# Kernel tuning notes

Measured on AMD Instinct MI355X. Metric: run time of the kernel, lower is better.

## Reference

```python
import jax, jax.numpy as jnp
import numpy as np

N_NODES = 100000
N_EDGES = 1600000
IN_DIM = 128
HID_DIM = 64
OUT_DIM = 1


def setup_inputs() -> dict:
    key = jax.random.key(0)
    k = jax.random.split(key, 8)
    x = jax.random.normal(k[0], (N_NODES, IN_DIM), dtype=jnp.float32)
    edge_index = jax.random.randint(k[1], (2, N_EDGES), 0, N_NODES, dtype=jnp.int64)
    # GCNConv layer 1: weight [IN, HID], bias [HID] (glorot-ish scale)
    W1 = jax.random.normal(k[2], (IN_DIM, HID_DIM), dtype=jnp.float32) / np.sqrt(IN_DIM)
    b1 = jnp.zeros((HID_DIM,), dtype=jnp.float32)
    W2 = jax.random.normal(k[3], (HID_DIM, HID_DIM), dtype=jnp.float32) / np.sqrt(HID_DIM)
    b2 = jnp.zeros((HID_DIM,), dtype=jnp.float32)
    Wfc = jax.random.normal(k[4], (HID_DIM, OUT_DIM), dtype=jnp.float32) / np.sqrt(HID_DIM)
    bfc = jnp.zeros((OUT_DIM,), dtype=jnp.float32)
    return {"x": x, "edge_index": edge_index, "W1": W1, "b1": b1,
            "W2": W2, "b2": b2, "Wfc": Wfc, "bfc": bfc}


def _gcn_norm(edge_index, n_nodes):
    # PyG GCNConv default: add self-loops, symmetric normalization.
    src, dst = edge_index[0], edge_index[1]
    loop = jnp.arange(n_nodes, dtype=src.dtype)
    src = jnp.concatenate([src, loop])
    dst = jnp.concatenate([dst, loop])
    deg = jax.ops.segment_sum(jnp.ones_like(dst, dtype=jnp.float32), dst,
                              num_segments=n_nodes)
    deg_isqrt = jax.lax.rsqrt(deg)  # deg >= 1 thanks to self-loops
    norm = deg_isqrt[src] * deg_isqrt[dst]  # [E+N]
    return src, dst, norm


def _gcn_conv(x, src, dst, norm, W, b, n_nodes):
    h = x @ W                      # [N, D_out] dense transform first (D_out <= D_in)
    msg = h[src] * norm[:, None]   # gather + normalize  [E+N, D_out]
    out = jax.ops.segment_sum(msg, dst, num_segments=n_nodes)  # scatter-add
    return out + b


def reference(x, edge_index, W1, b1, W2, b2, Wfc, bfc):
    n = x.shape[0]
    src, dst, norm = _gcn_norm(edge_index, n)
    h = jax.nn.relu(_gcn_conv(x, src, dst, norm, W1, b1, n))
    h = jax.nn.relu(_gcn_conv(h, src, dst, norm, W2, b2, n))
    return h @ Wfc + bfc  # [N, 1]
```

## Files before the change

kernel.cpp:

```cpp
#include <hip/hip_runtime.h>


#define IN_DIM 128
#define HID 64
#define B1 256
#define MAXNC 512

typedef unsigned int uint;
typedef unsigned short ushort;
typedef __attribute__((ext_vector_type(8))) short short8;
typedef __attribute__((ext_vector_type(4))) float f32x4;

__device__ inline uint pack_bf16x2(float a, float b) {
    uint ua = __builtin_bit_cast(uint, a);
    uint ub = __builtin_bit_cast(uint, b);
    ua += 0x7fffu + ((ua >> 16) & 1u);
    ub += 0x7fffu + ((ub >> 16) & 1u);
    return (ua >> 16) | (ub & 0xffff0000u);
}
__device__ inline float bf_lo(uint g) { return __builtin_bit_cast(float, g << 16); }
__device__ inline float bf_hi(uint g) { return __builtin_bit_cast(float, g & 0xffff0000u); }
__device__ inline uint rne_hi_bits(float a) {
    uint u = __builtin_bit_cast(uint, a);
    return (u + 0x7fffu + ((u >> 16) & 1u)) & 0xffff0000u;
}
__device__ inline float bitf(uint u) { return __builtin_bit_cast(float, u); }

__global__ __launch_bounds__(512) void hist1(const int* __restrict__ dst,
                                             int* __restrict__ ghist,
                                             int E, int NC, int chunk) {
    __shared__ int h[MAXNC];
    int t = threadIdx.x, blk = blockIdx.x;
    if (t < NC) h[t] = 0;
    __syncthreads();
    int s = blk * chunk, e = min(E, s + chunk);
    for (int i = s + t; i < e; i += 512) atomicAdd(&h[dst[i] >> 8], 1);
    __syncthreads();
    if (t < NC) ghist[(size_t)t * B1 + blk] = h[t];
}

__global__ __launch_bounds__(512) void scan_p12(const int* __restrict__ a,
                                                int* __restrict__ boff,
                                                int* __restrict__ row_off,
                                                int M, int N,
                                                const float* __restrict__ W1f,
                                                const float* __restrict__ W2f,
                                                ushort* __restrict__ w1h,
                                                ushort* __restrict__ w1l,
                                                ushort* __restrict__ w2h,
                                                ushort* __restrict__ w2l) {
    int t = threadIdx.x;
    {
        int c = t & 63;
        int kb1 = (t >> 6) * 16;
#pragma unroll 4
        for (int kk = 0; kk < 16; ++kk) {
            int k = kb1 + kk;
            float v = W1f[k * 64 + c];
            uint rh = rne_hi_bits(v);
            w1h[c * 128 + k] = (ushort)(rh >> 16);
            w1l[c * 128 + k] = (ushort)(rne_hi_bits(v - bitf(rh)) >> 16);
        }
        int kb2 = (t >> 6) * 8;
#pragma unroll 4
        for (int kk = 0; kk < 8; ++kk) {
            int k = kb2 + kk;
            float v = W2f[k * 64 + c];
            uint rh = rne_hi_bits(v);
            w2h[c * 64 + k] = (ushort)(rh >> 16);
            w2l[c * 64 + k] = (ushort)(rne_hi_bits(v - bitf(rh)) >> 16);
        }
    }
    const int nb = (M + 255) >> 8;
    int v = 0;
    if (t < nb) {
        int base = t * 256, end = min(M, base + 256);
        const int4* p4 = (const int4*)(a + base);
        int4 sa = make_int4(0, 0, 0, 0);
        int q4 = (end - base) >> 2;
        for (int k = 0; k < q4; ++k) {
            int4 q = p4[k];
            sa.x += q.x; sa.y += q.y; sa.z += q.z; sa.w += q.w;
        }
        v = sa.x + sa.y + sa.z + sa.w;
        for (int r = base + (q4 << 2); r < end; ++r) v += a[r];
    }
    __shared__ int s[512];
    s[t] = v;
    __syncthreads();
#pragma unroll
    for (int o = 1; o < 512; o <<= 1) {
        int add = (t >= o) ? s[t - o] : 0;
        __syncthreads();
        s[t] += add;
        __syncthreads();
    }
    if (t < nb) boff[t] = s[t] - v;
    if (t == nb - 1) row_off[N] = s[t];
}

__global__ __launch_bounds__(256) void scan_p3(int* __restrict__ a,
                                               const int* __restrict__ boff, int M) {
    __shared__ int s[256];
    int i = blockIdx.x * 256 + threadIdx.x;
    int t = threadIdx.x;
    int d = (i < M) ? a[i] : 0;
    s[t] = d;
    __syncthreads();
#pragma unroll
    for (int o = 1; o < 256; o <<= 1) {
        int add = (t >= o) ? s[t - o] : 0;
        __syncthreads();
        s[t] += add;
        __syncthreads();
    }
    if (i < M) a[i] = s[t] - d + boff[blockIdx.x];
}

__global__ __launch_bounds__(512) void scatter1(const int* __restrict__ src,
                                                const int* __restrict__ dst,
                                                const int* __restrict__ goff,
                                                uint* __restrict__ pairs,
                                                int E, int NC, int chunk) {
    __shared__ int cur[MAXNC];
    int t = threadIdx.x, blk = blockIdx.x;
    if (t < NC) cur[t] = goff[(size_t)t * B1 + blk];
    __syncthreads();
    int s = blk * chunk, e = min(E, s + chunk);
    for (int i = s + t; i < e; i += 512) {
        int d = dst[i];
        int p = atomicAdd(&cur[d >> 8], 1);
        pairs[p] = ((uint)src[i] << 8) | (uint)(d & 255);
    }
}

__global__ __launch_bounds__(256) void build_csr(const uint* __restrict__ pairs,
                                                 const int* __restrict__ goff,
                                                 int* __restrict__ row_off,
                                                 float* __restrict__ disqrt,
                                                 int* __restrict__ col,
                                                 int E, int NC, int N) {
    __shared__ int h[256], cur[256];
    __shared__ int ws[4], wsoff[4];
    int b = blockIdx.x, t = threadIdx.x;
    int base = goff[(size_t)b * B1];
    int next = (b + 1 < NC) ? goff[(size_t)(b + 1) * B1] : E;
    h[t] = 0;
    __syncthreads();
    for (int i = base + t; i < next; i += 256)
        atomicAdd(&h[pairs[i] & 255u], 1);
    __syncthreads();
    int deg = h[t];
    int incl = deg;
#pragma unroll
    for (int o = 1; o < 64; o <<= 1) {
        int u = __shfl_up(incl, o, 64);
        if ((t & 63) >= o) incl += u;
    }
    if ((t & 63) == 63) ws[t >> 6] = incl;
    __syncthreads();
    if (t == 0) {
        int run = 0;
#pragma unroll
        for (int i = 0; i < 4; ++i) { wsoff[i] = run; run += ws[i]; }
    }
    __syncthreads();
    int excl = wsoff[t >> 6] + incl - deg;
    cur[t] = base + excl;
    int node = (b << 8) + t;
    if (node < N) {
        row_off[node] = base + excl;
        disqrt[node]  = rsqrtf((float)(deg + 1));
    }
    __syncthreads();
    for (int i = base + t; i < next; i += 256) {
        uint p = pairs[i];
        int pos = atomicAdd(&cur[p & 255u], 1);
        col[pos] = (int)(p >> 8);
    }
}

template <int K, bool SPLIT>
__global__ __launch_bounds__(256) void gemm_mfma(const void* __restrict__ Xv,
                                                 const ushort* __restrict__ WHt,
                                                 const ushort* __restrict__ WLt,
                                                 const float* __restrict__ disqrt,
                                                 uint* __restrict__ Tsb, int n) {
    __shared__ ushort XH[128 * 40];
    __shared__ ushort WH[64 * 40];
    __shared__ ushort WL[64 * 40];
    __shared__ ushort XL[SPLIT ? 128 * 40 : 64];

    const int tid = threadIdx.x;
    const int m0  = blockIdx.x * 128;
    const float* Xf = (const float*)Xv;
    const char*  Xb = (const char*)Xv;

    const int wc = tid >> 2, wslot = tid & 3;
    const char* wh_g = (const char*)WHt + wc * (K * 2) + wslot * 16;
    const char* wl_g = (const char*)WLt + wc * (K * 2) + wslot * 16;

    constexpr int NL = SPLIT ? 4 : 2;
    int xr[NL], xk[NL];
#pragma unroll
    for (int i = 0; i < NL; ++i) {
        int f = tid + i * 256;
        if (SPLIT) { xr[i] = f >> 3; xk[i] = f & 7; }
        else       { xr[i] = f >> 2; xk[i] = f & 3; }
    }

    const float4 z4 = make_float4(0.f, 0.f, 0.f, 0.f);
    const uint4  zu = make_uint4(0u, 0u, 0u, 0u);
    float4 gx[NL];
    uint4  gxb[NL];
    uint4  gwh, gwl;
#pragma unroll
    for (int i = 0; i < NL; ++i) {
        int row = m0 + xr[i];
        if (SPLIT) gx[i]  = (row < n) ? *(const float4*)(Xf + (size_t)row * K + 4 * xk[i]) : z4;
        else       gxb[i] = (row < n) ? *(const uint4*)(Xb + (size_t)row * (K * 2) + xk[i] * 16) : zu;
    }
    gwh = *(const uint4*)wh_g;
    gwl = *(const uint4*)wl_g;

    f32x4 acc[2][4] = {};
    const int l   = tid & 63, wv = tid >> 6;
    const int lr  = l & 15;
    const int kob = (l >> 4) * 16;

    for (int kc = 0;;) {
        if (SPLIT) {
#pragma unroll
            for (int i = 0; i < NL; ++i) {
                float a = gx[i].x, b = gx[i].y, c = gx[i].z, d = gx[i].w;
                uint rha = rne_hi_bits(a), rhb = rne_hi_bits(b);
                uint rhc = rne_hi_bits(c), rhd = rne_hi_bits(d);
                uint2 hh, ll;
                hh.x = (rha >> 16) | (rhb & 0xffff0000u);
                hh.y = (rhc >> 16) | (rhd & 0xffff0000u);
                ll.x = pack_bf16x2(a - bitf(rha), b - bitf(rhb));
                ll.y = pack_bf16x2(c - bitf(rhc), d - bitf(rhd));
                *(uint2*)((char*)XH + xr[i] * 80 + xk[i] * 8) = hh;
                *(uint2*)((char*)XL + xr[i] * 80 + xk[i] * 8) = ll;
            }
        } else {
#pragma unroll
            for (int i = 0; i < NL; ++i)
                *(uint4*)((char*)XH + xr[i] * 80 + xk[i] * 16) = gxb[i];
        }
        *(uint4*)((char*)WH + wc * 80 + wslot * 16) = gwh;
        *(uint4*)((char*)WL + wc * 80 + wslot * 16) = gwl;
        __syncthreads();

        kc += 32;
        const bool more = kc < K;
        if (more) {
#pragma unroll
            for (int i = 0; i < NL; ++i) {
                int row = m0 + xr[i];
                if (SPLIT) gx[i]  = (row < n) ? *(const float4*)(Xf + (size_t)row * K + kc + 4 * xk[i]) : z4;
                else       gxb[i] = (row < n) ? *(const uint4*)(Xb + (size_t)row * (K * 2) + kc * 2 + xk[i] * 16) : zu;
            }
            gwh = *(const uint4*)(wh_g + kc * 2);
            gwl = *(const uint4*)(wl_g + kc * 2);
        }

        short8 xh0 = *(const short8*)((const char*)XH + (wv * 32 + 0 + lr) * 80 + kob);
        short8 xh1 = *(const short8*)((const char*)XH + (wv * 32 + 16 + lr) * 80 + kob);
        short8 xl0, xl1;
        if (SPLIT) {
            xl0 = *(const short8*)((const char*)XL + (wv * 32 + 0 + lr) * 80 + kob);
            xl1 = *(const short8*)((const char*)XL + (wv * 32 + 16 + lr) * 80 + kob);
        }
#pragma unroll
        for (int nn = 0; nn < 4; ++nn) {
            short8 wh = *(const short8*)((const char*)WH + (nn * 16 + lr) * 80 + kob);
            short8 wl = *(const short8*)((const char*)WL + (nn * 16 + lr) * 80 + kob);
            acc[0][nn] = __builtin_amdgcn_mfma_f32_16x16x32_bf16(wh, xh0, acc[0][nn], 0, 0, 0);
            acc[1][nn] = __builtin_amdgcn_mfma_f32_16x16x32_bf16(wh, xh1, acc[1][nn], 0, 0, 0);
            acc[0][nn] = __builtin_amdgcn_mfma_f32_16x16x32_bf16(wl, xh0, acc[0][nn], 0, 0, 0);
            acc[1][nn] = __builtin_amdgcn_mfma_f32_16x16x32_bf16(wl, xh1, acc[1][nn], 0, 0, 0);
            if (SPLIT) {
                acc[0][nn] = __builtin_amdgcn_mfma_f32_16x16x32_bf16(wh, xl0, acc[0][nn], 0, 0, 0);
                acc[1][nn] = __builtin_amdgcn_mfma_f32_16x16x32_bf16(wh, xl1, acc[1][nn], 0, 0, 0);
            }
        }
        if (!more) break;
        __syncthreads();
    }

#pragma unroll
    for (int m = 0; m < 2; ++m) {
        int node = m0 + wv * 32 + m * 16 + lr;
        if (node < n) {
            float dq = disqrt[node];
#pragma unroll
            for (int nn = 0; nn < 4; ++nn) {
                f32x4 a = acc[m][nn];
                uint2 pk;
                pk.x = pack_bf16x2(a[0] * dq, a[1] * dq);
                pk.y = pack_bf16x2(a[2] * dq, a[3] * dq);
                *(uint2*)((char*)Tsb + (size_t)node * 128 + nn * 32 + (l >> 4) * 8) = pk;
            }
        }
    }
}

template <bool FUSE_FC>
__global__ __launch_bounds__(256) void agg_kernel(const uint* __restrict__ Tsb,
                                                  const int* __restrict__ row_off,
                                                  const int* __restrict__ col,
                                                  const float* __restrict__ disqrt,
                                                  const float* __restrict__ bias,
                                                  const float* __restrict__ wfc,
                                                  const float* __restrict__ bfc,
                                                  uint* __restrict__ outb,
                                                  float* __restrict__ outf,
                                                  int node0, int nhi) {
    int node = node0 + blockIdx.x * 4 + (threadIdx.x >> 6);
    if (node >= nhi) return;
    int lane = threadIdx.x & 63;
    int o = lane >> 3;
    int p = lane & 7;
    float acc[8] = {};
    if (o == 0) {
        uint4 g = *(const uint4*)(Tsb + (size_t)node * 32 + 4 * p);
        acc[0] = bf_lo(g.x); acc[1] = bf_hi(g.x);
        acc[2] = bf_lo(g.y); acc[3] = bf_hi(g.y);
        acc[4] = bf_lo(g.z); acc[5] = bf_hi(g.z);
        acc[6] = bf_lo(g.w); acc[7] = bf_hi(g.w);
    }
    int beg = __builtin_amdgcn_readfirstlane(row_off[node]);
    int end = __builtin_amdgcn_readfirstlane(row_off[node + 1]);
    for (int batch = beg; batch < end; batch += 64) {
        int bn = min(64, end - batch);
        int cv = 0;
        if (batch + lane < end) cv = col[batch + lane];
        int j = 0;
        for (; j + 16 <= bn; j += 16) {
            int s0 = __shfl(cv, j + o, 64);
            int s1 = __shfl(cv, j + 8 + o, 64);
            uint4 g0 = *(const uint4*)(Tsb + (size_t)s0 * 32 + 4 * p);
            uint4 g1 = *(const uint4*)(Tsb + (size_t)s1 * 32 + 4 * p);
            acc[0] += bf_lo(g0.x); acc[1] += bf_hi(g0.x);
            acc[2] += bf_lo(g0.y); acc[3] += bf_hi(g0.y);
            acc[4] += bf_lo(g0.z); acc[5] += bf_hi(g0.z);
            acc[6] += bf_lo(g0.w); acc[7] += bf_hi(g0.w);
            acc[0] += bf_lo(g1.x); acc[1] += bf_hi(g1.x);
            acc[2] += bf_lo(g1.y); acc[3] += bf_hi(g1.y);
            acc[4] += bf_lo(g1.z); acc[5] += bf_hi(g1.z);
            acc[6] += bf_lo(g1.w); acc[7] += bf_hi(g1.w);
        }
        for (; j < bn; j += 8) {
            int idx = j + o;
            int s = __shfl(cv, idx & 63, 64);
            uint4 g = *(const uint4*)(Tsb + (size_t)s * 32 + 4 * p);
            if (idx < bn) {
                acc[0] += bf_lo(g.x); acc[1] += bf_hi(g.x);
                acc[2] += bf_lo(g.y); acc[3] += bf_hi(g.y);
                acc[4] += bf_lo(g.z); acc[5] += bf_hi(g.z);
                acc[6] += bf_lo(g.w); acc[7] += bf_hi(g.w);
            }
        }
    }
#pragma unroll
    for (int k = 0; k < 8; ++k) {
        acc[k] += __shfl_xor(acc[k], 8, 64);
        acc[k] += __shfl_xor(acc[k], 16, 64);
        acc[k] += __shfl_xor(acc[k], 32, 64);
    }
    float dq = disqrt[node];
    float4 bv0 = *(const float4*)(bias + 8 * p);
    float4 bv1 = *(const float4*)(bias + 8 * p + 4);
    float r[8];
    r[0] = fmaxf(acc[0] * dq + bv0.x, 0.f);
    r[1] = fmaxf(acc[1] * dq + bv0.y, 0.f);
    r[2] = fmaxf(acc[2] * dq + bv0.z, 0.f);
    r[3] = fmaxf(acc[3] * dq + bv0.w, 0.f);
    r[4] = fmaxf(acc[4] * dq + bv1.x, 0.f);
    r[5] = fmaxf(acc[5] * dq + bv1.y, 0.f);
    r[6] = fmaxf(acc[6] * dq + bv1.z, 0.f);
    r[7] = fmaxf(acc[7] * dq + bv1.w, 0.f);
    if (!FUSE_FC) {
        if (o == 0) {
            uint4 pk;
            pk.x = pack_bf16x2(r[0], r[1]);
            pk.y = pack_bf16x2(r[2], r[3]);
            pk.z = pack_bf16x2(r[4], r[5]);
            pk.w = pack_bf16x2(r[6], r[7]);
            *(uint4*)(outb + (size_t)node * 32 + 4 * p) = pk;
        }
    } else {
        float4 wv0 = *(const float4*)(wfc + 8 * p);
        float4 wv1 = *(const float4*)(wfc + 8 * p + 4);
        float v = r[0] * wv0.x + r[1] * wv0.y + r[2] * wv0.z + r[3] * wv0.w +
                  r[4] * wv1.x + r[5] * wv1.y + r[6] * wv1.z + r[7] * wv1.w;
        v += __shfl_down(v, 4, 64);
        v += __shfl_down(v, 2, 64);
        v += __shfl_down(v, 1, 64);
        if (lane == 0) outf[node] = v + bfc[0];
    }
}

extern "C" void kernel_launch(void* const* d_in, const int* in_sizes, int n_in,
                              void* d_out, int out_size, void* d_ws, size_t ws_size,
                              hipStream_t stream) {
    const float* x   = (const float*)d_in[0];
    const int*   ei  = (const int*)d_in[1];
    const float* W1  = (const float*)d_in[2];
    const float* b1  = (const float*)d_in[3];
    const float* W2  = (const float*)d_in[4];
    const float* b2  = (const float*)d_in[5];
    const float* Wfc = (const float*)d_in[6];
    const float* bfc = (const float*)d_in[7];
    float* out = (float*)d_out;

    const int N = in_sizes[0] / IN_DIM;
    const int E = in_sizes[1] / 2;
    const int* src = ei;
    const int* dst = ei + E;
    const int NC    = (N + 255) >> 8;
    const int chunk = (E + B1 - 1) / B1;
    const int M     = NC * B1;
    const int NBs   = (M + 255) / 256;

    char* w = (char*)d_ws;
    auto alloc = [&](size_t bytes) {
        void* p = (void*)w;
        w += (bytes + 255) & ~(size_t)255;
        return p;
    };
    int*   row_off = (int*)alloc((size_t)(N + 1) * 4);
    float* disqrt  = (float*)alloc((size_t)N * 4);
    int*   goff    = (int*)alloc((size_t)NC * B1 * 4);
    int*   boff    = (int*)alloc(512 * 4);
    int*   col     = (int*)alloc((size_t)E * 4);
    ushort* w1h    = (ushort*)alloc(64 * 128 * 2);
    ushort* w1l    = (ushort*)alloc(64 * 128 * 2);
    ushort* w2h    = (ushort*)alloc(64 * 64 * 2);
    ushort* w2l    = (ushort*)alloc(64 * 64 * 2);
    size_t scrA = (size_t)E * 4, scrB = (size_t)N * HID * 2;
    void*  scr  = alloc(scrA > scrB ? scrA : scrB);
    uint*  h1b  = (uint*)alloc((size_t)N * HID * 2);
    uint*  pairs = (uint*)scr;
    uint*  Tsb   = (uint*)scr;

    hist1<<<B1, 512, 0, stream>>>(dst, goff, E, NC, chunk);
    scan_p12<<<1, 512, 0, stream>>>(goff, boff, row_off, M, N,
                                    W1, W2, w1h, w1l, w2h, w2l);
    scan_p3<<<NBs, 256, 0, stream>>>(goff, boff, M);
    scatter1<<<B1, 512, 0, stream>>>(src, dst, goff, pairs, E, NC, chunk);
    build_csr<<<NC, 256, 0, stream>>>(pairs, goff, row_off, disqrt, col, E, NC, N);

    const int H = ((N + 7) / 8) * 4;

    gemm_mfma<IN_DIM, true><<<(N + 127) / 128, 256, 0, stream>>>(
        x, w1h, w1l, disqrt, Tsb, N);
    agg_kernel<false><<<(H + 3) / 4, 256, 0, stream>>>(Tsb, row_off, col, disqrt,
                                                       b1, nullptr, nullptr,
                                                       h1b, nullptr, 0, H);
    agg_kernel<false><<<(N - H + 3) / 4, 256, 0, stream>>>(Tsb, row_off, col, disqrt,
                                                           b1, nullptr, nullptr,
                                                           h1b, nullptr, H, N);

    gemm_mfma<HID, false><<<(N + 127) / 128, 256, 0, stream>>>(
        h1b, w2h, w2l, disqrt, Tsb, N);
    agg_kernel<true><<<(H + 3) / 4, 256, 0, stream>>>(Tsb, row_off, col, disqrt,
                                                      b2, Wfc, bfc,
                                                      nullptr, out, 0, H);
    agg_kernel<true><<<(N - H + 3) / 4, 256, 0, stream>>>(Tsb, row_off, col, disqrt,
                                                          b2, Wfc, bfc,
                                                          nullptr, out, H, N);
}
```

Before: 283.8 us.

## Replace two-level bucketed CSR build with global-atomic degree histogram and scatter

Drops the staged CSR construction (bucket histogram, bucket scatter of packed pairs, then per-bucket local sort) and replaces it with direct global atomics: a per-node degree histogram, a scan that produces row offsets, cursors and inverse square-root degrees, and a scatter that writes each source index through an atomic cursor. The aggregation launches are also merged from two half-range launches into one each. This removes a pass over the edges and the intermediate pairs buffer, but uses global atomics on 100k counters, which can contend. It also writes the columns of each row in nondeterministic order, which may hurt gather locality in aggregation.

```diff
diff --git a/kernel.cpp b/kernel.cpp
--- a/kernel.cpp
+++ b/kernel.cpp
@@ -3,8 +3,6 @@
 
 #define IN_DIM 128
 #define HID 64
-#define B1 256
-#define MAXNC 512
 
 typedef unsigned int uint;
 typedef unsigned short ushort;
@@ -26,17 +24,20 @@
 }
 __device__ inline float bitf(uint u) { return __builtin_bit_cast(float, u); }
 
-__global__ __launch_bounds__(512) void hist1(const int* __restrict__ dst,
-                                             int* __restrict__ ghist,
-                                             int E, int NC, int chunk) {
-    __shared__ int h[MAXNC];
-    int t = threadIdx.x, blk = blockIdx.x;
-    if (t < NC) h[t] = 0;
-    __syncthreads();
-    int s = blk * chunk, e = min(E, s + chunk);
-    for (int i = s + t; i < e; i += 512) atomicAdd(&h[dst[i] >> 8], 1);
-    __syncthreads();
-    if (t < NC) ghist[(size_t)t * B1 + blk] = h[t];
+__global__ __launch_bounds__(256) void deg_hist(const int* __restrict__ dst,
+                                                int* __restrict__ deg, int E) {
+    int i = blockIdx.x * 256 + threadIdx.x;
+    int q = E >> 2;
+    const int4* d4 = (const int4*)dst;
+    for (int k = i; k < q; k += gridDim.x * 256) {
+        int4 v = d4[k];
+        atomicAdd(&deg[v.x], 1);
+        atomicAdd(&deg[v.y], 1);
+        atomicAdd(&deg[v.z], 1);
+        atomicAdd(&deg[v.w], 1);
+    }
+    for (int k = (q << 2) + i; k < E; k += gridDim.x * 256)
+        atomicAdd(&deg[dst[k]], 1);
 }
 
 __global__ __launch_bounds__(512) void scan_p12(const int* __restrict__ a,
@@ -99,12 +100,15 @@
     if (t == nb - 1) row_off[N] = s[t];
 }
 
-__global__ __launch_bounds__(256) void scan_p3(int* __restrict__ a,
-                                               const int* __restrict__ boff, int M) {
+__global__ __launch_bounds__(256) void scan_p3(const int* __restrict__ deg,
+                                               const int* __restrict__ boff,
+                                               int* __restrict__ row_off,
+                                               int* __restrict__ cur,
+                                               float* __restrict__ disqrt, int N) {
     __shared__ int s[256];
     int i = blockIdx.x * 256 + threadIdx.x;
     int t = threadIdx.x;
-    int d = (i < M) ? a[i] : 0;
+    int d = (i < N) ? deg[i] : 0;
     s[t] = d;
     __syncthreads();
 #pragma unroll
@@ -114,70 +118,32 @@
         s[t] += add;
         __syncthreads();
     }
-    if (i < M) a[i] = s[t] - d + boff[blockIdx.x];
-}
-
-__global__ __launch_bounds__(512) void scatter1(const int* __restrict__ src,
-                                                const int* __restrict__ dst,
-                                                const int* __restrict__ goff,
-                                                uint* __restrict__ pairs,
-                                                int E, int NC, int chunk) {
-    __shared__ int cur[MAXNC];
-    int t = threadIdx.x, blk = blockIdx.x;
-    if (t < NC) cur[t] = goff[(size_t)t * B1 + blk];
-    __syncthreads();
-    int s = blk * chunk, e = min(E, s + chunk);
-    for (int i = s + t; i < e; i += 512) {
-        int d = dst[i];
-        int p = atomicAdd(&cur[d >> 8], 1);
-        pairs[p] = ((uint)src[i] << 8) | (uint)(d & 255);
-    }
-}
-
-__global__ __launch_bounds__(256) void build_csr(const uint* __restrict__ pairs,
-                                                 const int* __restrict__ goff,
-                                                 int* __restrict__ row_off,
-                                                 float* __restrict__ disqrt,
-                                                 int* __restrict__ col,
-                                                 int E, int NC, int N) {
-    __shared__ int h[256], cur[256];
-    __shared__ int ws[4], wsoff[4];
-    int b = blockIdx.x, t = threadIdx.x;
-    int base = goff[(size_t)b * B1];
-    int next = (b + 1 < NC) ? goff[(size_t)(b + 1) * B1] : E;
-    h[t] = 0;
-    __syncthreads();
-    for (int i = base + t; i < next; i += 256)
-        atomicAdd(&h[pairs[i] & 255u], 1);
-    __syncthreads();
-    int deg = h[t];
-    int incl = deg;
-#pragma unroll
-    for (int o = 1; o < 64; o <<= 1) {
-        int u = __shfl_up(incl, o, 64);
-        if ((t & 63) >= o) incl += u;
-    }
-    if ((t & 63) == 63) ws[t >> 6] = incl;
-    __syncthreads();
-    if (t == 0) {
-        int run = 0;
-#pragma unroll
-        for (int i = 0; i < 4; ++i) { wsoff[i] = run; run += ws[i]; }
-    }
-    __syncthreads();
-    int excl = wsoff[t >> 6] + incl - deg;
-    cur[t] = base + excl;
-    int node = (b << 8) + t;
-    if (node < N) {
-        row_off[node] = base + excl;
-        disqrt[node]  = rsqrtf((float)(deg + 1));
-    }
-    __syncthreads();
-    for (int i = base + t; i < next; i += 256) {
-        uint p = pairs[i];
-        int pos = atomicAdd(&cur[p & 255u], 1);
-        col[pos] = (int)(p >> 8);
-    }
+    if (i < N) {
+        int ex = s[t] - d + boff[blockIdx.x];
+        row_off[i] = ex;
+        cur[i]     = ex;
+        disqrt[i]  = rsqrtf((float)(d + 1));
+    }
+}
+
+__global__ __launch_bounds__(256) void scatter_csr(const int* __restrict__ src,
+                                                   const int* __restrict__ dst,
+                                                   int* __restrict__ cur,
+                                                   int* __restrict__ col, int E) {
+    int i = blockIdx.x * 256 + threadIdx.x;
+    int q = E >> 2;
+    const int4* s4 = (const int4*)src;
+    const int4* d4 = (const int4*)dst;
+    for (int k = i; k < q; k += gridDim.x * 256) {
+        int4 d = d4[k];
+        int4 s = s4[k];
+        col[atomicAdd(&cur[d.x], 1)] = s.x;
+        col[atomicAdd(&cur[d.y], 1)] = s.y;
+        col[atomicAdd(&cur[d.z], 1)] = s.z;
+        col[atomicAdd(&cur[d.w], 1)] = s.w;
+    }
+    for (int k = (q << 2) + i; k < E; k += gridDim.x * 256)
+        col[atomicAdd(&cur[dst[k]], 1)] = src[k];
 }
 
 template <int K, bool SPLIT>
@@ -419,10 +385,7 @@
     const int E = in_sizes[1] / 2;
     const int* src = ei;
     const int* dst = ei + E;
-    const int NC    = (N + 255) >> 8;
-    const int chunk = (E + B1 - 1) / B1;
-    const int M     = NC * B1;
-    const int NBs   = (M + 255) / 256;
+    const int NBs = (N + 255) / 256;
 
     char* w = (char*)d_ws;
     auto alloc = [&](size_t bytes) {
@@ -432,43 +395,33 @@
     };
     int*   row_off = (int*)alloc((size_t)(N + 1) * 4);
     float* disqrt  = (float*)alloc((size_t)N * 4);
-    int*   goff    = (int*)alloc((size_t)NC * B1 * 4);
+    int*   deg     = (int*)alloc((size_t)N * 4);
+    int*   cur     = (int*)alloc((size_t)N * 4);
     int*   boff    = (int*)alloc(512 * 4);
     int*   col     = (int*)alloc((size_t)E * 4);
     ushort* w1h    = (ushort*)alloc(64 * 128 * 2);
     ushort* w1l    = (ushort*)alloc(64 * 128 * 2);
     ushort* w2h    = (ushort*)alloc(64 * 64 * 2);
     ushort* w2l    = (ushort*)alloc(64 * 64 * 2);
-    size_t scrA = (size_t)E * 4, scrB = (size_t)N * HID * 2;
-    void*  scr  = alloc(scrA > scrB ? scrA : scrB);
-    uint*  h1b  = (uint*)alloc((size_t)N * HID * 2);
-    uint*  pairs = (uint*)scr;
-    uint*  Tsb   = (uint*)scr;
-
-    hist1<<<B1, 512, 0, stream>>>(dst, goff, E, NC, chunk);
-    scan_p12<<<1, 512, 0, stream>>>(goff, boff, row_off, M, N,
+    uint*  Tsb     = (uint*)alloc((size_t)N * HID * 2);
+    uint*  h1b     = (uint*)alloc((size_t)N * HID * 2);
+
+    hipMemsetAsync(deg, 0, (size_t)N * 4, stream);
+    deg_hist<<<1024, 256, 0, stream>>>(dst, deg, E);
+    scan_p12<<<1, 512, 0, stream>>>(deg, boff, row_off, N, N,
                                     W1, W2, w1h, w1l, w2h, w2l);
-    scan_p3<<<NBs, 256, 0, stream>>>(goff, boff, M);
-    scatter1<<<B1, 512, 0, stream>>>(src, dst, goff, pairs, E, NC, chunk);
-    build_csr<<<NC, 256, 0, stream>>>(pairs, goff, row_off, disqrt, col, E, NC, N);
-
-    const int H = ((N + 7) / 8) * 4;
+    scan_p3<<<NBs, 256, 0, stream>>>(deg, boff, row_off, cur, disqrt, N);
+    scatter_csr<<<1024, 256, 0, stream>>>(src, dst, cur, col, E);
 
     gemm_mfma<IN_DIM, true><<<(N + 127) / 128, 256, 0, stream>>>(
         x, w1h, w1l, disqrt, Tsb, N);
-    agg_kernel<false><<<(H + 3) / 4, 256, 0, stream>>>(Tsb, row_off, col, disqrt,
+    agg_kernel<false><<<(N + 3) / 4, 256, 0, stream>>>(Tsb, row_off, col, disqrt,
                                                        b1, nullptr, nullptr,
-                                                       h1b, nullptr, 0, H);
-    agg_kernel<false><<<(N - H + 3) / 4, 256, 0, stream>>>(Tsb, row_off, col, disqrt,
-                                                           b1, nullptr, nullptr,
-                                                           h1b, nullptr, H, N);
+                                                       h1b, nullptr, 0, N);
 
     gemm_mfma<HID, false><<<(N + 127) / 128, 256, 0, stream>>>(
         h1b, w2h, w2l, disqrt, Tsb, N);
-    agg_kernel<true><<<(H + 3) / 4, 256, 0, stream>>>(Tsb, row_off, col, disqrt,
+    agg_kernel<true><<<(N + 3) / 4, 256, 0, stream>>>(Tsb, row_off, col, disqrt,
                                                       b2, Wfc, bfc,
-                                                      nullptr, out, 0, H);
-    agg_kernel<true><<<(N - H + 3) / 4, 256, 0, stream>>>(Tsb, row_off, col, disqrt,
-                                                          b2, Wfc, bfc,
-                                                          nullptr, out, H, N);
-}
+                                                      nullptr, out, 0, N);
+}
```

New measurement: 424.7 us. 1.5x slower.
